# Performance work log

Measured on AMD Instinct MI355X. Metric: run time of the kernel, lower is better.

## Reference

```python
import jax, jax.numpy as jnp
import numpy as np

B, C_IN, H, W = 16, 256, 64, 64
D_LAT = 256
K = 4096


def setup_inputs() -> dict:
    key = jax.random.key(0)
    k1, k2, k3, k4 = jax.random.split(key, 4)
    z = jax.random.normal(k1, (B, C_IN, H, W), dtype=jnp.float32)
    # 1x1 conv weight (out=latent, in=hidden), fan-in scaled
    proj_w = jax.random.normal(k2, (D_LAT, C_IN), dtype=jnp.float32) / np.sqrt(C_IN)
    proj_b = jax.random.normal(k3, (D_LAT,), dtype=jnp.float32) * 0.01
    # codebook init: uniform(-1/K, 1/K) as in init_weights
    emb = (jax.random.uniform(k4, (K, D_LAT), dtype=jnp.float32) * 2.0 - 1.0) / K
    return {"z": z, "proj_w": proj_w, "proj_b": proj_b, "emb": emb}


def reference(z, proj_w, proj_b, emb):
    # 1x1 conv == channel-wise matmul
    zp = jnp.einsum('bchw,oc->bohw', z, proj_w) + proj_b[None, :, None, None]
    zt = jnp.transpose(zp, (0, 2, 3, 1))          # [B,H,W,D]
    zf = zt.reshape(-1, D_LAT)                    # [N,D]
    # squared euclidean distance: ||z||^2 - 2 z.e + ||e||^2
    dist = ((zf * zf).sum(-1, keepdims=True)
            - 2.0 * (zf @ emb.T)
            + (emb * emb).sum(-1)[None, :])       # [N,K]
    idx = jnp.argmin(dist, axis=1)                # [N]
    # one-hot @ emb == gather
    z_q = emb[idx].reshape(zt.shape)              # [B,H,W,D]
    rep = zt + jax.lax.stop_gradient(z_q - zt)    # straight-through
    return jnp.transpose(rep, (0, 3, 1, 2))       # [B,D,H,W]
```

## Files before the change

kernel.cpp:

```cpp
#include <hip/hip_runtime.h>
#include <math.h>

#define NTOT  65536
#define DLAT  256
#define KCB   4096
#define CIN   256
#define HWSZ  4096

#define OFF_ZPT   0u
#define OFF_EMBT  16777216u
#define OFF_WT    17825792u
#define OFF_ENORM 17891328u
#define OFF_RNORM 17895424u
#define OFF_IDX   17960960u

__global__ __launch_bounds__(256) void wt_kernel(const float* __restrict__ w, float* __restrict__ wT) {
    int t = blockIdx.x * 256 + threadIdx.x;
    int o = t >> 8, c = t & 255;
    wT[c * 256 + o] = w[t];
}

__global__ __launch_bounds__(256) void et_kernel(const float* __restrict__ emb, float* __restrict__ embT) {
    int t = blockIdx.x * 256 + threadIdx.x;
    int k = t >> 8, d = t & 255;
    embT[d * KCB + k] = emb[t];
}

__global__ __launch_bounds__(64) void enorm_kernel(const float* __restrict__ emb, float* __restrict__ enorm) {
    int k = blockIdx.x;
    int lane = threadIdx.x;
    double a = 0.0;
    #pragma unroll
    for (int i = 0; i < 4; ++i) {
        float v = emb[k * DLAT + lane + i * 64];
        a = fma((double)v, (double)v, a);
    }
    #pragma unroll
    for (int off = 32; off > 0; off >>= 1) a += __shfl_down(a, off);
    if (lane == 0) enorm[k] = (float)a;
}

__global__ __launch_bounds__(256) void rnorm_kernel(const float* __restrict__ zpT, float* __restrict__ rnorm) {
    int n = blockIdx.x * 256 + threadIdx.x;
    double a = 0.0;
    for (int o = 0; o < DLAT; ++o) {
        float v = zpT[(size_t)o * NTOT + n];
        a = fma((double)v, (double)v, a);
    }
    rnorm[n] = (float)a;
}

__global__ __launch_bounds__(256) void proj_kernel(const float* __restrict__ z, const float* __restrict__ wT,
                                                   const float* __restrict__ bias, float* __restrict__ zpT) {
    __shared__ float zT[16][128];
    __shared__ float wt[16][64];
    int n0 = blockIdx.x * 128;
    int o0 = blockIdx.y * 64;
    int t = threadIdx.x;
    int tm = t & 15, tn = t >> 4;
    int b = n0 >> 12;
    int hw0 = n0 & 4095;
    float acc[8][4] = {};
    for (int c0 = 0; c0 < CIN; c0 += 16) {
        __syncthreads();
        #pragma unroll
        for (int i = 0; i < 2; ++i) {
            int e4 = t + i * 256;
            int cc = e4 >> 5, c4 = e4 & 31;
            float4 v = *(const float4*)(z + (size_t)(b * CIN + c0 + cc) * HWSZ + hw0 + c4 * 4);
            *(float4*)&zT[cc][c4 * 4] = v;
        }
        {
            int cc = t >> 4, c4 = t & 15;
            float4 v = *(const float4*)(wT + (size_t)(c0 + cc) * 256 + o0 + c4 * 4);
            *(float4*)&wt[cc][c4 * 4] = v;
        }
        __syncthreads();
        #pragma unroll
        for (int d = 0; d < 16; ++d) {
            float4 a0 = *(const float4*)&zT[d][tm * 8];
            float4 a1 = *(const float4*)&zT[d][tm * 8 + 4];
            float4 bv = *(const float4*)&wt[d][tn * 4];
            float a[8] = {a0.x,a0.y,a0.z,a0.w,a1.x,a1.y,a1.z,a1.w};
            float bb[4] = {bv.x,bv.y,bv.z,bv.w};
            #pragma unroll
            for (int i = 0; i < 8; ++i)
                #pragma unroll
                for (int j = 0; j < 4; ++j)
                    acc[i][j] = fmaf(a[i], bb[j], acc[i][j]);
        }
    }
    #pragma unroll
    for (int j = 0; j < 4; ++j) {
        int o = o0 + tn * 4 + j;
        float bv = bias[o];
        #pragma unroll
        for (int i = 0; i < 8; ++i) {
            int n = n0 + tm * 8 + i;
            zpT[(size_t)o * NTOT + n] = acc[i][j] + bv;
        }
    }
}

__global__ __launch_bounds__(256) void argmin_kernel(const float* __restrict__ zpT, const float* __restrict__ embT,
                                                     const float* __restrict__ enorm, const float* __restrict__ rnorm,
                                                     int* __restrict__ idx) {
    __shared__ float zT[16][128];
    __shared__ float eT[16][64];
    __shared__ float en_s[64];
    __shared__ float rv[128][17];
    __shared__ int   ri[128][17];
    int n0 = blockIdx.x * 128;
    int t = threadIdx.x;
    int tm = t & 15, tn = t >> 4;
    float best[8];
    int bidx[8];
    float rn[8];
    #pragma unroll
    for (int i = 0; i < 8; ++i) {
        best[i] = INFINITY; bidx[i] = 0;
        rn[i] = rnorm[n0 + tm * 8 + i];
    }
    for (int k0 = 0; k0 < KCB; k0 += 64) {
        __syncthreads();
        if (t < 64) en_s[t] = enorm[k0 + t];
        float acc[8][4] = {};
        for (int d0 = 0; d0 < DLAT; d0 += 16) {
            if (d0) __syncthreads();
            #pragma unroll
            for (int i = 0; i < 2; ++i) {
                int e4 = t + i * 256;
                int cc = e4 >> 5, c4 = e4 & 31;
                float4 v = *(const float4*)(zpT + (size_t)(d0 + cc) * NTOT + n0 + c4 * 4);
                *(float4*)&zT[cc][c4 * 4] = v;
            }
            {
                int cc = t >> 4, c4 = t & 15;
                float4 v = *(const float4*)(embT + (size_t)(d0 + cc) * KCB + k0 + c4 * 4);
                *(float4*)&eT[cc][c4 * 4] = v;
            }
            __syncthreads();
            float cacc[8][4] = {};
            #pragma unroll
            for (int d = 0; d < 16; ++d) {
                float4 a0 = *(const float4*)&zT[d][tm * 8];
                float4 a1 = *(const float4*)&zT[d][tm * 8 + 4];
                float4 bv = *(const float4*)&eT[d][tn * 4];
                float a[8] = {a0.x,a0.y,a0.z,a0.w,a1.x,a1.y,a1.z,a1.w};
                float bb[4] = {bv.x,bv.y,bv.z,bv.w};
                #pragma unroll
                for (int i = 0; i < 8; ++i)
                    #pragma unroll
                    for (int j = 0; j < 4; ++j)
                        cacc[i][j] = fmaf(a[i], bb[j], cacc[i][j]);
            }
            #pragma unroll
            for (int i = 0; i < 8; ++i)
                #pragma unroll
                for (int j = 0; j < 4; ++j)
                    acc[i][j] += cacc[i][j];
        }
        #pragma unroll
        for (int j = 0; j < 4; ++j) {
            int g = k0 + tn * 4 + j;
            float en = en_s[tn * 4 + j];
            #pragma unroll
            for (int i = 0; i < 8; ++i) {
                float s1 = rn[i] - 2.0f * acc[i][j];
                float dist = s1 + en;
                if (dist < best[i]) { best[i] = dist; bidx[i] = g; }
            }
        }
    }
    __syncthreads();
    #pragma unroll
    for (int i = 0; i < 8; ++i) {
        rv[tm * 8 + i][tn] = best[i];
        ri[tm * 8 + i][tn] = bidx[i];
    }
    __syncthreads();
    if (t < 128) {
        float bv = rv[t][0]; int bi = ri[t][0];
        #pragma unroll
        for (int q = 1; q < 16; ++q) {
            float v = rv[t][q]; int iq = ri[t][q];
            if (v < bv || (v == bv && iq < bi)) { bv = v; bi = iq; }
        }
        idx[n0 + t] = bi;
    }
}

__global__ __launch_bounds__(256) void out_kernel(const float* __restrict__ zpT, const float* __restrict__ emb,
                                                  const int* __restrict__ idx, float* __restrict__ out) {
    int e = blockIdx.x * 256 + threadIdx.x;
    int hw = e & 4095;
    int o = (e >> 12) & 255;
    int b = e >> 20;
    int n = (b << 12) | hw;
    float zp = zpT[(size_t)o * NTOT + n];
    float ev = emb[idx[n] * DLAT + o];
    float st = ev - zp;
    out[e] = zp + st;
}

extern "C" void kernel_launch(void* const* d_in, const int* in_sizes, int n_in,
                              void* d_out, int out_size, void* d_ws, size_t ws_size,
                              hipStream_t stream) {
    const float* z    = (const float*)d_in[0];
    const float* w    = (const float*)d_in[1];
    const float* bias = (const float*)d_in[2];
    const float* emb  = (const float*)d_in[3];
    float* ws = (float*)d_ws;
    float* zpT   = ws + OFF_ZPT;
    float* embT  = ws + OFF_EMBT;
    float* wT    = ws + OFF_WT;
    float* enorm = ws + OFF_ENORM;
    float* rnorm = ws + OFF_RNORM;
    int*   idx   = (int*)(ws + OFF_IDX);
    float* out   = (float*)d_out;

    hipLaunchKernelGGL(wt_kernel,     dim3(256),      dim3(256), 0, stream, w, wT);
    hipLaunchKernelGGL(et_kernel,     dim3(4096),     dim3(256), 0, stream, emb, embT);
    hipLaunchKernelGGL(enorm_kernel,  dim3(4096),     dim3(64),  0, stream, emb, enorm);
    hipLaunchKernelGGL(proj_kernel,   dim3(512, 4),   dim3(256), 0, stream, z, wT, bias, zpT);
    hipLaunchKernelGGL(rnorm_kernel,  dim3(256),      dim3(256), 0, stream, zpT, rnorm);
    hipLaunchKernelGGL(argmin_kernel, dim3(512),      dim3(256), 0, stream, zpT, embT, enorm, rnorm, idx);
    hipLaunchKernelGGL(out_kernel,    dim3(65536),    dim3(256), 0, stream, zpT, emb, idx, out);
}
```

Before: 2.440 ms.

## Restructure argmin as register-tiled per-thread rows with split-K codebook and merge

Replaces the shared-memory tiled distance GEMM with a kernel where each thread owns two rows and 32 codebook entries in registers. Codebook values are read as wave-uniform scalar loads from global memory, with no LDS and no block barriers. The codebook is split into four slices across a second grid dimension, and a new merge kernel reduces the per-slice candidates to the final index. The cost is a high register count (64+ accumulators plus partials) and lower occupancy. The merge also keeps the earlier slice on ties, which preserves lowest-index tie-breaking.

Result: slower. 3.143 ms (+28.8%).

```diff
diff --git a/kernel.cpp b/kernel.cpp
--- a/kernel.cpp
+++ b/kernel.cpp
@@ -13,6 +13,8 @@
 #define OFF_ENORM 17891328u
 #define OFF_RNORM 17895424u
 #define OFF_IDX   17960960u
+#define OFF_CD    18026496u
+#define OFF_CI    18288640u
 
 __global__ __launch_bounds__(256) void wt_kernel(const float* __restrict__ w, float* __restrict__ wT) {
     int t = blockIdx.x * 256 + threadIdx.x;
@@ -104,90 +106,67 @@
 
 __global__ __launch_bounds__(256) void argmin_kernel(const float* __restrict__ zpT, const float* __restrict__ embT,
                                                      const float* __restrict__ enorm, const float* __restrict__ rnorm,
-                                                     int* __restrict__ idx) {
-    __shared__ float zT[16][128];
-    __shared__ float eT[16][64];
-    __shared__ float en_s[64];
-    __shared__ float rv[128][17];
-    __shared__ int   ri[128][17];
-    int n0 = blockIdx.x * 128;
-    int t = threadIdx.x;
-    int tm = t & 15, tn = t >> 4;
-    float best[8];
-    int bidx[8];
-    float rn[8];
-    #pragma unroll
-    for (int i = 0; i < 8; ++i) {
-        best[i] = INFINITY; bidx[i] = 0;
-        rn[i] = rnorm[n0 + tm * 8 + i];
-    }
-    for (int k0 = 0; k0 < KCB; k0 += 64) {
-        __syncthreads();
-        if (t < 64) en_s[t] = enorm[k0 + t];
-        float acc[8][4] = {};
+                                                     float* __restrict__ cand_d, int* __restrict__ cand_i) {
+    const int lane = threadIdx.x & 63;
+    const int wv = threadIdx.x >> 6;
+    const int row0 = blockIdx.x * 512 + wv * 128 + lane * 2;
+    const int s = blockIdx.y;
+    const int ksplit = s * 1024;
+    const float2 rnv = *(const float2*)(rnorm + row0);
+    const float* __restrict__ ap = zpT + row0;
+    float best0 = INFINITY, best1 = INFINITY;
+    int bi0 = 0, bi1 = 0;
+    for (int p = 0; p < 32; ++p) {
+        const int kbase = ksplit + p * 32;
+        float acc0[32], acc1[32];
+        #pragma unroll
+        for (int k = 0; k < 32; ++k) { acc0[k] = 0.0f; acc1[k] = 0.0f; }
         for (int d0 = 0; d0 < DLAT; d0 += 16) {
-            if (d0) __syncthreads();
-            #pragma unroll
-            for (int i = 0; i < 2; ++i) {
-                int e4 = t + i * 256;
-                int cc = e4 >> 5, c4 = e4 & 31;
-                float4 v = *(const float4*)(zpT + (size_t)(d0 + cc) * NTOT + n0 + c4 * 4);
-                *(float4*)&zT[cc][c4 * 4] = v;
+            float c0[32], c1[32];
+            #pragma unroll
+            for (int k = 0; k < 32; ++k) { c0[k] = 0.0f; c1[k] = 0.0f; }
+            #pragma unroll
+            for (int dd = 0; dd < 16; ++dd) {
+                const int d = d0 + dd;
+                const float2 av = *(const float2*)(ap + (size_t)d * NTOT);
+                const float* __restrict__ eb = embT + (size_t)d * KCB + kbase;
+                #pragma unroll
+                for (int k = 0; k < 32; ++k) {
+                    const float bv = eb[k];
+                    c0[k] = fmaf(av.x, bv, c0[k]);
+                    c1[k] = fmaf(av.y, bv, c1[k]);
+                }
             }
-            {
-                int cc = t >> 4, c4 = t & 15;
-                float4 v = *(const float4*)(embT + (size_t)(d0 + cc) * KCB + k0 + c4 * 4);
-                *(float4*)&eT[cc][c4 * 4] = v;
-            }
-            __syncthreads();
-            float cacc[8][4] = {};
-            #pragma unroll
-            for (int d = 0; d < 16; ++d) {
-                float4 a0 = *(const float4*)&zT[d][tm * 8];
-                float4 a1 = *(const float4*)&zT[d][tm * 8 + 4];
-                float4 bv = *(const float4*)&eT[d][tn * 4];
-                float a[8] = {a0.x,a0.y,a0.z,a0.w,a1.x,a1.y,a1.z,a1.w};
-                float bb[4] = {bv.x,bv.y,bv.z,bv.w};
-                #pragma unroll
-                for (int i = 0; i < 8; ++i)
-                    #pragma unroll
-                    for (int j = 0; j < 4; ++j)
-                        cacc[i][j] = fmaf(a[i], bb[j], cacc[i][j]);
-            }
-            #pragma unroll
-            for (int i = 0; i < 8; ++i)
-                #pragma unroll
-                for (int j = 0; j < 4; ++j)
-                    acc[i][j] += cacc[i][j];
-        }
-        #pragma unroll
-        for (int j = 0; j < 4; ++j) {
-            int g = k0 + tn * 4 + j;
-            float en = en_s[tn * 4 + j];
-            #pragma unroll
-            for (int i = 0; i < 8; ++i) {
-                float s1 = rn[i] - 2.0f * acc[i][j];
-                float dist = s1 + en;
-                if (dist < best[i]) { best[i] = dist; bidx[i] = g; }
-            }
-        }
-    }
-    __syncthreads();
-    #pragma unroll
-    for (int i = 0; i < 8; ++i) {
-        rv[tm * 8 + i][tn] = best[i];
-        ri[tm * 8 + i][tn] = bidx[i];
-    }
-    __syncthreads();
-    if (t < 128) {
-        float bv = rv[t][0]; int bi = ri[t][0];
-        #pragma unroll
-        for (int q = 1; q < 16; ++q) {
-            float v = rv[t][q]; int iq = ri[t][q];
-            if (v < bv || (v == bv && iq < bi)) { bv = v; bi = iq; }
-        }
-        idx[n0 + t] = bi;
-    }
+            #pragma unroll
+            for (int k = 0; k < 32; ++k) { acc0[k] += c0[k]; acc1[k] += c1[k]; }
+        }
+        const float* __restrict__ ep = enorm + kbase;
+        #pragma unroll
+        for (int k = 0; k < 32; ++k) {
+            const float en = ep[k];
+            const float dv0 = (rnv.x - 2.0f * acc0[k]) + en;
+            const float dv1 = (rnv.y - 2.0f * acc1[k]) + en;
+            const int g = kbase + k;
+            if (dv0 < best0) { best0 = dv0; bi0 = g; }
+            if (dv1 < best1) { best1 = dv1; bi1 = g; }
+        }
+    }
+    *(float2*)(cand_d + s * NTOT + row0) = make_float2(best0, best1);
+    *(int2*)(cand_i + s * NTOT + row0) = make_int2(bi0, bi1);
+}
+
+__global__ __launch_bounds__(256) void merge_kernel(const float* __restrict__ cand_d, const int* __restrict__ cand_i,
+                                                    int* __restrict__ idx) {
+    int n = blockIdx.x * 256 + threadIdx.x;
+    float bv = cand_d[n];
+    int bi = cand_i[n];
+    #pragma unroll
+    for (int s = 1; s < 4; ++s) {
+        float v = cand_d[s * NTOT + n];
+        int iv = cand_i[s * NTOT + n];
+        if (v < bv) { bv = v; bi = iv; }
+    }
+    idx[n] = bi;
 }
 
 __global__ __launch_bounds__(256) void out_kernel(const float* __restrict__ zpT, const float* __restrict__ emb,
@@ -217,6 +196,8 @@
     float* enorm = ws + OFF_ENORM;
     float* rnorm = ws + OFF_RNORM;
     int*   idx   = (int*)(ws + OFF_IDX);
+    float* cand_d = ws + OFF_CD;
+    int*   cand_i = (int*)(ws + OFF_CI);
     float* out   = (float*)d_out;
 
     hipLaunchKernelGGL(wt_kernel,     dim3(256),      dim3(256), 0, stream, w, wT);
@@ -224,6 +205,7 @@
     hipLaunchKernelGGL(enorm_kernel,  dim3(4096),     dim3(64),  0, stream, emb, enorm);
     hipLaunchKernelGGL(proj_kernel,   dim3(512, 4),   dim3(256), 0, stream, z, wT, bias, zpT);
     hipLaunchKernelGGL(rnorm_kernel,  dim3(256),      dim3(256), 0, stream, zpT, rnorm);
-    hipLaunchKernelGGL(argmin_kernel, dim3(512),      dim3(256), 0, stream, zpT, embT, enorm, rnorm, idx);
+    hipLaunchKernelGGL(argmin_kernel, dim3(128, 4),   dim3(256), 0, stream, zpT, embT, enorm, rnorm, cand_d, cand_i);
+    hipLaunchKernelGGL(merge_kernel,  dim3(256),      dim3(256), 0, stream, cand_d, cand_i, idx);
     hipLaunchKernelGGL(out_kernel,    dim3(65536),    dim3(256), 0, stream, zpT, emb, idx, out);
 }
```

## Enlarge argmin tile to 128x128 with 8x8 microtiles and register prefetch

Applied to the files above, without the earlier changes.

The argmin GEMM now works on a 128-codeword by 128-row tile per block, with each thread computing an 8x8 microtile instead of 8x4. Global loads for the next k/d slice are prefetched into registers while the current slice is computed. The loop over k and d is flattened into one loop, and codebook norms are read straight from global memory. The aim is better arithmetic intensity and hiding of global-load latency, at the cost of much higher register pressure (64 accumulators plus 64 partial sums), which could reduce occupancy or cause spills.

New measurement: 2.048 ms. 16.1% less time.

```diff
diff --git a/kernel.cpp b/kernel.cpp
--- a/kernel.cpp
+++ b/kernel.cpp
@@ -106,77 +106,90 @@
                                                      const float* __restrict__ enorm, const float* __restrict__ rnorm,
                                                      int* __restrict__ idx) {
     __shared__ float zT[16][128];
-    __shared__ float eT[16][64];
-    __shared__ float en_s[64];
+    __shared__ float eT[16][128];
     __shared__ float rv[128][17];
     __shared__ int   ri[128][17];
-    int n0 = blockIdx.x * 128;
-    int t = threadIdx.x;
-    int tm = t & 15, tn = t >> 4;
-    float best[8];
-    int bidx[8];
+    const int t = threadIdx.x;
+    const int tm = t & 15, tn = t >> 4;
+    const int n0 = blockIdx.x * 128;
+    const int sdd0 = t >> 5;
+    const int sdd1 = sdd0 + 8;
+    const int sc0 = (t & 31) * 4;
+
     float rn[8];
     #pragma unroll
-    for (int i = 0; i < 8; ++i) {
-        best[i] = INFINITY; bidx[i] = 0;
-        rn[i] = rnorm[n0 + tm * 8 + i];
-    }
-    for (int k0 = 0; k0 < KCB; k0 += 64) {
-        __syncthreads();
-        if (t < 64) en_s[t] = enorm[k0 + t];
-        float acc[8][4] = {};
-        for (int d0 = 0; d0 < DLAT; d0 += 16) {
-            if (d0) __syncthreads();
-            #pragma unroll
-            for (int i = 0; i < 2; ++i) {
-                int e4 = t + i * 256;
-                int cc = e4 >> 5, c4 = e4 & 31;
-                float4 v = *(const float4*)(zpT + (size_t)(d0 + cc) * NTOT + n0 + c4 * 4);
-                *(float4*)&zT[cc][c4 * 4] = v;
-            }
-            {
-                int cc = t >> 4, c4 = t & 15;
-                float4 v = *(const float4*)(embT + (size_t)(d0 + cc) * KCB + k0 + c4 * 4);
-                *(float4*)&eT[cc][c4 * 4] = v;
-            }
-            __syncthreads();
-            float cacc[8][4] = {};
-            #pragma unroll
-            for (int d = 0; d < 16; ++d) {
-                float4 a0 = *(const float4*)&zT[d][tm * 8];
-                float4 a1 = *(const float4*)&zT[d][tm * 8 + 4];
-                float4 bv = *(const float4*)&eT[d][tn * 4];
-                float a[8] = {a0.x,a0.y,a0.z,a0.w,a1.x,a1.y,a1.z,a1.w};
-                float bb[4] = {bv.x,bv.y,bv.z,bv.w};
-                #pragma unroll
-                for (int i = 0; i < 8; ++i)
-                    #pragma unroll
-                    for (int j = 0; j < 4; ++j)
-                        cacc[i][j] = fmaf(a[i], bb[j], cacc[i][j]);
-            }
+    for (int i = 0; i < 4; ++i) {
+        rn[i]     = rnorm[n0 + tm * 4 + i];
+        rn[4 + i] = rnorm[n0 + 64 + tm * 4 + i];
+    }
+    float best[8]; int bidx[8];
+    #pragma unroll
+    for (int i = 0; i < 8; ++i) { best[i] = INFINITY; bidx[i] = 0; }
+
+    float acc[64];
+    float4 gA0 = *(const float4*)(zpT + (size_t)sdd0 * NTOT + n0 + sc0);
+    float4 gA1 = *(const float4*)(zpT + (size_t)sdd1 * NTOT + n0 + sc0);
+    float4 gB0 = *(const float4*)(embT + (size_t)sdd0 * KCB + sc0);
+    float4 gB1 = *(const float4*)(embT + (size_t)sdd1 * KCB + sc0);
+
+    for (int u = 0; u < 512; ++u) {
+        if ((u & 15) == 0) {
+            #pragma unroll
+            for (int x = 0; x < 64; ++x) acc[x] = 0.0f;
+        }
+        __syncthreads();
+        *(float4*)&zT[sdd0][sc0] = gA0;
+        *(float4*)&zT[sdd1][sc0] = gA1;
+        *(float4*)&eT[sdd0][sc0] = gB0;
+        *(float4*)&eT[sdd1][sc0] = gB1;
+        if (u < 511) {
+            const int un = u + 1;
+            const int k0n = (un >> 4) << 7;
+            const int d0n = (un & 15) << 4;
+            gA0 = *(const float4*)(zpT + (size_t)(d0n + sdd0) * NTOT + n0 + sc0);
+            gA1 = *(const float4*)(zpT + (size_t)(d0n + sdd1) * NTOT + n0 + sc0);
+            gB0 = *(const float4*)(embT + (size_t)(d0n + sdd0) * KCB + k0n + sc0);
+            gB1 = *(const float4*)(embT + (size_t)(d0n + sdd1) * KCB + k0n + sc0);
+        }
+        __syncthreads();
+        float cacc[64];
+        #pragma unroll
+        for (int x = 0; x < 64; ++x) cacc[x] = 0.0f;
+        #pragma unroll
+        for (int dd = 0; dd < 16; ++dd) {
+            float4 a0 = *(const float4*)&zT[dd][tm * 4];
+            float4 a1 = *(const float4*)&zT[dd][64 + tm * 4];
+            float4 b0 = *(const float4*)&eT[dd][tn * 8];
+            float4 b1 = *(const float4*)&eT[dd][tn * 8 + 4];
+            float a[8] = {a0.x,a0.y,a0.z,a0.w,a1.x,a1.y,a1.z,a1.w};
+            float b[8] = {b0.x,b0.y,b0.z,b0.w,b1.x,b1.y,b1.z,b1.w};
             #pragma unroll
             for (int i = 0; i < 8; ++i)
                 #pragma unroll
-                for (int j = 0; j < 4; ++j)
-                    acc[i][j] += cacc[i][j];
-        }
-        #pragma unroll
-        for (int j = 0; j < 4; ++j) {
-            int g = k0 + tn * 4 + j;
-            float en = en_s[tn * 4 + j];
-            #pragma unroll
-            for (int i = 0; i < 8; ++i) {
-                float s1 = rn[i] - 2.0f * acc[i][j];
-                float dist = s1 + en;
-                if (dist < best[i]) { best[i] = dist; bidx[i] = g; }
+                for (int j = 0; j < 8; ++j)
+                    cacc[i * 8 + j] = fmaf(a[i], b[j], cacc[i * 8 + j]);
+        }
+        #pragma unroll
+        for (int x = 0; x < 64; ++x) acc[x] += cacc[x];
+        if ((u & 15) == 15) {
+            const int k0 = (u >> 4) << 7;
+            #pragma unroll
+            for (int j = 0; j < 8; ++j) {
+                const int g = k0 + tn * 8 + j;
+                const float en = enorm[g];
+                #pragma unroll
+                for (int i = 0; i < 8; ++i) {
+                    const float dv = (rn[i] - 2.0f * acc[i * 8 + j]) + en;
+                    if (dv < best[i]) { best[i] = dv; bidx[i] = g; }
+                }
             }
         }
     }
     __syncthreads();
     #pragma unroll
-    for (int i = 0; i < 8; ++i) {
-        rv[tm * 8 + i][tn] = best[i];
-        ri[tm * 8 + i][tn] = bidx[i];
+    for (int i = 0; i < 4; ++i) {
+        rv[tm * 4 + i][tn] = best[i];          ri[tm * 4 + i][tn] = bidx[i];
+        rv[64 + tm * 4 + i][tn] = best[4 + i]; ri[64 + tm * 4 + i][tn] = bidx[4 + i];
     }
     __syncthreads();
     if (t < 128) {
```
